# Kernel optimization log

Hardware: AMD Instinct MI355X
Metric: run time of the kernel (lower is better)

Reference implementation:

```python
import jax, jax.numpy as jnp
import numpy as np

# Straight-through-estimator round (round_pass in the original code)
def _round_ste(x):
    return x + jax.lax.stop_gradient(jnp.round(x) - x)

INPUT_QMAX = 127.0   # 2**(input_bit-1)-1,  input_bit=8
WEIGHT_QMAX = 127.0  # 2**(weight_bit-1)-1, weight_bit=8
OUT_RANGE = 127.0    # 2**(output_bit-1)-1, output_bit=8


def setup_inputs() -> dict:
    key = jax.random.key(0)
    k0, k1, k2 = jax.random.split(key, 3)
    B, Cin, Cout, H, W, K = 16, 320, 320, 64, 64, 3
    x = jax.random.normal(k0, (B, Cin, H, W), dtype=jnp.float32)
    weight = jax.random.normal(k1, (Cout, Cin, K, K), dtype=jnp.float32) * 0.05
    bias = jax.random.normal(k2, (Cout,), dtype=jnp.float32) * 0.1
    # LSQ learned scalar step sizes (cloned from conv_lsq in the original)
    step_x = jnp.float32(0.02)
    step_w = jnp.float32(0.002)
    step_b = jnp.float32(0.01)
    # Bit_shift_layer scale: shift conv accumulator down into output_bit range
    shift_scale = jnp.float32(2.0 ** -7)
    return {"x": x, "weight": weight, "bias": bias, "step_x": step_x,
            "step_w": step_w, "step_b": step_b, "shift_scale": shift_scale}


def reference(x, weight, bias, step_x, step_w, step_b, shift_scale):
    # --- lsq_quant_input (isint=True): x_int in [-127,127], x_scale = 1/step ---
    x_int = jnp.clip(_round_ste(x / step_x), -INPUT_QMAX, INPUT_QMAX)
    x_scale = 1.0 / step_x
    # --- lsq_quant_weight (isint=True) ---
    w_int = jnp.clip(_round_ste(weight / step_w), -WEIGHT_QMAX, WEIGHT_QMAX)
    w_scale = 1.0 / step_w
    # --- Conv2d_int: integer-valued conv (no bias) ---
    y_int = jax.lax.conv_general_dilated(
        x_int, w_int, window_strides=(1, 1), padding=((1, 1), (1, 1)),
        dimension_numbers=("NCHW", "OIHW", "NCHW"))
    # --- mvm_result_shift: bit-shift accumulator into output range ---
    y_shift = jnp.clip(_round_ste(y_int * shift_scale), -OUT_RANGE, OUT_RANGE)
    # --- lsq_quant_bias (isint=False): dequantized bias ---
    b_deq = jnp.clip(_round_ste(bias / step_b), -OUT_RANGE, OUT_RANGE) * step_b
    # --- bias requant to output int scale, add, clamp (fused epilogue) ---
    b_int8 = jnp.clip(_round_ste(b_deq * shift_scale * x_scale * w_scale),
                      -OUT_RANGE, OUT_RANGE)
    y_shift_dmac = jnp.clip(y_shift + b_int8[None, :, None, None],
                            -OUT_RANGE, OUT_RANGE)
    # module returns y_shift_DMAC (the integer-valued clamped output)
    return y_shift_dmac
```

## Files before the change

kernel.cpp:

```cpp
#include <hip/hip_runtime.h>

typedef int v4i __attribute__((ext_vector_type(4)));

#define QMAX 127.0f

#define XQ_BYTES 22302720
#define WQ_BYTES 921600

__device__ __forceinline__ float clampf(float v, float lo, float hi) {
    return fminf(fmaxf(v, lo), hi);
}

__device__ __forceinline__ void gload_lds16(const char* g, char* l) {
    __builtin_amdgcn_global_load_lds(
        (const __attribute__((address_space(1))) void*)g,
        (__attribute__((address_space(3))) void*)l, 16, 0, 0);
}

__global__ __launch_bounds__(256) void quant_x_kernel(
    const float* __restrict__ x, const float* __restrict__ step_p,
    char* __restrict__ xq)
{
    __shared__ float F[64 * 65];
    const int t   = threadIdx.x;
    const int ci0 = blockIdx.x * 64;
    const int h   = blockIdx.y;
    const int b   = blockIdx.z;
    const float step = *step_p;

    {
        const int r = t >> 2, q = t & 3;
        const float* src = x + (((size_t)(b * 320 + ci0 + r) * 64 + h) * 64);
#pragma unroll
        for (int i = 0; i < 4; ++i) {
            float4 v = *(const float4*)(src + q * 16 + i * 4);
            float* dst = &F[r * 65 + q * 16 + i * 4];
            dst[0] = v.x; dst[1] = v.y; dst[2] = v.z; dst[3] = v.w;
        }
    }
    __syncthreads();

    {
        const int w  = t & 63;
        const int cg = t >> 6;
        int dws[4];
#pragma unroll
        for (int j = 0; j < 4; ++j) {
            int word = 0;
#pragma unroll
            for (int k2 = 0; k2 < 4; ++k2) {
                int ci = cg * 16 + j * 4 + k2;
                float v = F[ci * 65 + w];
                int xi = (int)clampf(rintf(v / step), -QMAX, QMAX);
                word |= (xi & 0xFF) << (8 * k2);
            }
            dws[j] = word;
        }
        v4i pk = { dws[0], dws[1], dws[2], dws[3] };
        size_t off = ((size_t)(b * 66 + (h + 1)) * 66 + (w + 1)) * 320 + ci0 + cg * 16;
        *(v4i*)&xq[off] = pk;
    }
}

__global__ __launch_bounds__(256) void halo_kernel(char* __restrict__ xq)
{
    int tid = blockIdx.x * 256 + threadIdx.x;
    if (tid >= 83200) return;
    int b = tid / 5200;
    int r = tid - b * 5200;
    int px = r / 20;
    int ck = (r - px * 20) * 16;
    int row, col;
    if (px < 66)       { row = 0;  col = px; }
    else if (px < 132) { row = 65; col = px - 66; }
    else { int e = px - 132; row = 1 + (e >> 1); col = (e & 1) * 65; }
    size_t off = ((size_t)(b * 66 + row) * 66 + col) * 320 + ck;
    v4i z = {0, 0, 0, 0};
    *(v4i*)&xq[off] = z;
}

__global__ __launch_bounds__(256) void quant_w_kernel(
    const float* __restrict__ w, const float* __restrict__ step_p,
    char* __restrict__ wq2)
{
    int tid = blockIdx.x * 256 + threadIdx.x;
    const float step = *step_p;
    int co = tid / 320;
    int ci = tid - co * 320;
    int c5 = ci >> 6, quad = (ci >> 4) & 3, j = ci & 15;
    int cog = co >> 4, l15 = co & 15;
    const float* src = w + (size_t)co * 2880 + ci * 9;
    size_t base = ((size_t)(c5 * 20 + cog) * 64 + (l15 + quad * 16)) * 16 + j;
#pragma unroll
    for (int p = 0; p < 9; ++p) {
        float v = src[p];
        int q = (int)clampf(rintf(v / step), -QMAX, QMAX);
        wq2[p * 102400 + base] = (char)q;
    }
}

__global__ void quant_b_kernel(
    const float* __restrict__ bias, const float* __restrict__ step_b_p,
    const float* __restrict__ step_x_p, const float* __restrict__ step_w_p,
    const float* __restrict__ shift_p, float* __restrict__ bi)
{
    const int co = threadIdx.x;
    if (co >= 320) return;
    const float step_b = *step_b_p;
    const float xs = 1.0f / *step_x_p;
    const float ws = 1.0f / *step_w_p;
    const float shift = *shift_p;
    float b_deq = clampf(rintf(bias[co] / step_b), -QMAX, QMAX) * step_b;
    float v = ((b_deq * shift) * xs) * ws;
    bi[co] = clampf(rintf(v), -QMAX, QMAX);
}

__global__ __launch_bounds__(256) void conv_mfma_kernel(
    const char* __restrict__ xq, const char* __restrict__ wq2,
    const float* __restrict__ bi, const float* __restrict__ shift_p,
    float* __restrict__ out)
{
    __shared__ __attribute__((aligned(16))) char A_lds[36864];
    __shared__ __attribute__((aligned(16))) char B_lds[25344];

    const int t   = threadIdx.x;
    const int bx  = blockIdx.x;
    const int co0 = bx * 64;
    const int ptile = blockIdx.y;
    const int b  = ptile >> 4;
    const int h0 = (ptile & 15) * 4;

    const int wave = t >> 6, lane = t & 63;
    const int quad = lane >> 4, l15 = lane & 15;

    const char* xbase = xq + ((size_t)(b * 66 + h0) * 66) * 320;

    v4i acc[4][4] = {};

    for (int c5 = 0; c5 < 5; ++c5) {
        const int ci0 = c5 * 64;

        for (int c = t; c < 1584; c += 256) {
            int px = c >> 2;
            int ck = (c & 3) << 4;
            v4i v = *(const v4i*)&xbase[(size_t)px * 320 + ci0 + ck];
            *(v4i*)&B_lds[px * 64 + (ck ^ ((((px >> 1) & 3)) << 4))] = v;
        }

        {
            const char* g = wq2 + ((size_t)(c5 * 20 + bx * 4 + wave)) * 1024
                            + (size_t)lane * 16;
            char* l = &A_lds[wave * 1024];
#pragma unroll
            for (int p = 0; p < 9; ++p)
                gload_lds16(g + (size_t)p * 102400, l + p * 4096);
        }

        __syncthreads();

#pragma unroll
        for (int p = 0; p < 9; ++p) {
            const int dh = p / 3, dw = p - dh * 3;
            v4i a[4], bf[4];
#pragma unroll
            for (int cs = 0; cs < 4; ++cs)
                a[cs] = *(const v4i*)&A_lds[(p * 4 + cs) * 1024 + lane * 16];
#pragma unroll
            for (int i = 0; i < 4; ++i) {
                int px = (wave + dh) * 66 + i * 16 + l15 + dw;
                bf[i] = *(const v4i*)&B_lds[px * 64 +
                         ((quad << 4) ^ (((px >> 1) & 3) << 4))];
            }
#pragma unroll
            for (int cs = 0; cs < 4; ++cs)
#pragma unroll
                for (int i = 0; i < 4; ++i)
                    acc[cs][i] = __builtin_amdgcn_mfma_i32_16x16x64_i8(
                        a[cs], bf[i], acc[cs][i], 0, 0, 0);
        }

        __syncthreads();
    }

    const float shift = *shift_p;
    const int h = h0 + wave;
#pragma unroll
    for (int cs = 0; cs < 4; ++cs) {
#pragma unroll
        for (int reg = 0; reg < 4; ++reg) {
            const int co = co0 + cs * 16 + quad * 4 + reg;
            const float bv = bi[co];
            float* orow = out + (((size_t)(b * 320 + co) * 64) + h) * 64;
#pragma unroll
            for (int i = 0; i < 4; ++i) {
                float y  = (float)acc[cs][i][reg];
                float ys = clampf(rintf(y * shift), -QMAX, QMAX);
                orow[i * 16 + l15] = clampf(ys + bv, -QMAX, QMAX);
            }
        }
    }
}

extern "C" void kernel_launch(void* const* d_in, const int* in_sizes, int n_in,
                              void* d_out, int out_size, void* d_ws, size_t ws_size,
                              hipStream_t stream) {
    const float* x      = (const float*)d_in[0];
    const float* w      = (const float*)d_in[1];
    const float* bias   = (const float*)d_in[2];
    const float* step_x = (const float*)d_in[3];
    const float* step_w = (const float*)d_in[4];
    const float* step_b = (const float*)d_in[5];
    const float* shift  = (const float*)d_in[6];
    float* out = (float*)d_out;

    char*  xq  = (char*)d_ws;
    char*  wq2 = xq + XQ_BYTES;
    float* bi  = (float*)(wq2 + WQ_BYTES);

    quant_x_kernel<<<dim3(5, 64, 16), 256, 0, stream>>>(x, step_x, xq);
    halo_kernel<<<325, 256, 0, stream>>>(xq);
    quant_w_kernel<<<400, 256, 0, stream>>>(w, step_w, wq2);
    quant_b_kernel<<<1, 320, 0, stream>>>(bias, step_b, step_x, step_w, shift, bi);
    conv_mfma_kernel<<<dim3(5, 256), 256, 0, stream>>>(xq, wq2, bi, shift, out);
}
```

Measured before the change: 238.4 us.

## Double rows per conv tile, merge prep kernels, coalesce quant_x loads

```diff
diff --git a/kernel.cpp b/kernel.cpp
--- a/kernel.cpp
+++ b/kernel.cpp
@@ -15,6 +15,10 @@
     __builtin_amdgcn_global_load_lds(
         (const __attribute__((address_space(1))) void*)g,
         (__attribute__((address_space(3))) void*)l, 16, 0, 0);
+}
+
+__device__ __forceinline__ v4i mfma_i8(v4i a, v4i b, v4i c) {
+    return __builtin_amdgcn_mfma_i32_16x16x64_i8(a, b, c, 0, 0, 0);
 }
 
 __global__ __launch_bounds__(256) void quant_x_kernel(
@@ -29,13 +33,13 @@
     const float step = *step_p;
 
     {
-        const int r = t >> 2, q = t & 3;
-        const float* src = x + (((size_t)(b * 320 + ci0 + r) * 64 + h) * 64);
+        const int r = t >> 4, c = (t & 15) * 4;
+        const float* src = x + (((size_t)(b * 320 + ci0) * 64 + h) * 64);
 #pragma unroll
         for (int i = 0; i < 4; ++i) {
-            float4 v = *(const float4*)(src + q * 16 + i * 4);
-            float* dst = &F[r * 65 + q * 16 + i * 4];
-            dst[0] = v.x; dst[1] = v.y; dst[2] = v.z; dst[3] = v.w;
+            const int row = r + i * 16;
+            float4 v = *(const float4*)(src + (size_t)row * 4096 + c);
+            *(float4*)&F[row * 65 + c] = v;
         }
     }
     __syncthreads();
@@ -62,140 +66,142 @@
     }
 }
 
-__global__ __launch_bounds__(256) void halo_kernel(char* __restrict__ xq)
+__global__ __launch_bounds__(256) void prep_kernel(
+    const float* __restrict__ w, const float* __restrict__ bias,
+    const float* __restrict__ step_w_p, const float* __restrict__ step_b_p,
+    const float* __restrict__ step_x_p, const float* __restrict__ shift_p,
+    char* __restrict__ wq2, char* __restrict__ xq, float* __restrict__ bi)
 {
-    int tid = blockIdx.x * 256 + threadIdx.x;
-    if (tid >= 83200) return;
-    int b = tid / 5200;
-    int r = tid - b * 5200;
-    int px = r / 20;
-    int ck = (r - px * 20) * 16;
-    int row, col;
-    if (px < 66)       { row = 0;  col = px; }
-    else if (px < 132) { row = 65; col = px - 66; }
-    else { int e = px - 132; row = 1 + (e >> 1); col = (e & 1) * 65; }
-    size_t off = ((size_t)(b * 66 + row) * 66 + col) * 320 + ck;
-    v4i z = {0, 0, 0, 0};
-    *(v4i*)&xq[off] = z;
-}
-
-__global__ __launch_bounds__(256) void quant_w_kernel(
-    const float* __restrict__ w, const float* __restrict__ step_p,
-    char* __restrict__ wq2)
-{
-    int tid = blockIdx.x * 256 + threadIdx.x;
-    const float step = *step_p;
-    int co = tid / 320;
-    int ci = tid - co * 320;
-    int c5 = ci >> 6, quad = (ci >> 4) & 3, j = ci & 15;
-    int cog = co >> 4, l15 = co & 15;
-    const float* src = w + (size_t)co * 2880 + ci * 9;
-    size_t base = ((size_t)(c5 * 20 + cog) * 64 + (l15 + quad * 16)) * 16 + j;
-#pragma unroll
-    for (int p = 0; p < 9; ++p) {
-        float v = src[p];
+    const int bid = blockIdx.x;
+    if (bid < 3600) {
+        const int tid = bid * 256 + threadIdx.x;
+        const float step = *step_w_p;
+        const int p    = tid / 102400;
+        const int r    = tid - p * 102400;
+        const int c5   = r / 20480;
+        const int r2   = r - c5 * 20480;
+        const int cog  = r2 >> 10;
+        const int r3   = r2 & 1023;
+        const int lane = r3 >> 4, j = r3 & 15;
+        const int co = cog * 16 + (lane & 15);
+        const int ci = c5 * 64 + (lane >> 4) * 16 + j;
+        float v = w[(size_t)co * 2880 + ci * 9 + p];
         int q = (int)clampf(rintf(v / step), -QMAX, QMAX);
-        wq2[p * 102400 + base] = (char)q;
-    }
-}
-
-__global__ void quant_b_kernel(
-    const float* __restrict__ bias, const float* __restrict__ step_b_p,
-    const float* __restrict__ step_x_p, const float* __restrict__ step_w_p,
-    const float* __restrict__ shift_p, float* __restrict__ bi)
-{
-    const int co = threadIdx.x;
-    if (co >= 320) return;
-    const float step_b = *step_b_p;
-    const float xs = 1.0f / *step_x_p;
-    const float ws = 1.0f / *step_w_p;
-    const float shift = *shift_p;
-    float b_deq = clampf(rintf(bias[co] / step_b), -QMAX, QMAX) * step_b;
-    float v = ((b_deq * shift) * xs) * ws;
-    bi[co] = clampf(rintf(v), -QMAX, QMAX);
-}
-
-__global__ __launch_bounds__(256) void conv_mfma_kernel(
+        wq2[tid] = (char)q;
+    } else if (bid < 3925) {
+        int tid = (bid - 3600) * 256 + threadIdx.x;
+        if (tid < 83200) {
+            int b = tid / 5200;
+            int r = tid - b * 5200;
+            int px = r / 20;
+            int ck = (r - px * 20) * 16;
+            int row, col;
+            if (px < 66)       { row = 0;  col = px; }
+            else if (px < 132) { row = 65; col = px - 66; }
+            else { int e = px - 132; row = 1 + (e >> 1); col = (e & 1) * 65; }
+            size_t off = ((size_t)(b * 66 + row) * 66 + col) * 320 + ck;
+            v4i z = {0, 0, 0, 0};
+            *(v4i*)&xq[off] = z;
+        }
+    } else {
+        const float step_b = *step_b_p;
+        const float xs = 1.0f / *step_x_p;
+        const float ws = 1.0f / *step_w_p;
+        const float shift = *shift_p;
+#pragma unroll
+        for (int co = threadIdx.x; co < 320; co += 256) {
+            float b_deq = clampf(rintf(bias[co] / step_b), -QMAX, QMAX) * step_b;
+            float v = ((b_deq * shift) * xs) * ws;
+            bi[co] = clampf(rintf(v), -QMAX, QMAX);
+        }
+    }
+}
+
+template<int ROWS, int WAVES>
+__global__ __launch_bounds__(WAVES * 64, 2) void conv_mfma_kernel(
     const char* __restrict__ xq, const char* __restrict__ wq2,
     const float* __restrict__ bi, const float* __restrict__ shift_p,
     float* __restrict__ out)
 {
-    __shared__ __attribute__((aligned(16))) char A_lds[36864];
-    __shared__ __attribute__((aligned(16))) char B_lds[25344];
+    extern __shared__ __align__(16) char lds[];
+    char* B_lds = lds;
+    char* A_lds = lds + (ROWS + 2) * 66 * 64;
 
     const int t   = threadIdx.x;
     const int bx  = blockIdx.x;
     const int co0 = bx * 64;
     const int ptile = blockIdx.y;
-    const int b  = ptile >> 4;
-    const int h0 = (ptile & 15) * 4;
+    constexpr int TPI = 64 / ROWS;
+    const int b  = ptile / TPI;
+    const int h0 = (ptile % TPI) * ROWS;
 
     const int wave = t >> 6, lane = t & 63;
     const int quad = lane >> 4, l15 = lane & 15;
 
     const char* xbase = xq + ((size_t)(b * 66 + h0) * 66) * 320;
-
-    v4i acc[4][4] = {};
+    constexpr int BCHUNKS = (ROWS + 2) * 66 * 4;
+
+    v4i acc[4][8] = {};
 
     for (int c5 = 0; c5 < 5; ++c5) {
         const int ci0 = c5 * 64;
 
-        for (int c = t; c < 1584; c += 256) {
+        for (int c = t; c < BCHUNKS; c += WAVES * 64) {
             int px = c >> 2;
             int ck = (c & 3) << 4;
             v4i v = *(const v4i*)&xbase[(size_t)px * 320 + ci0 + ck];
             *(v4i*)&B_lds[px * 64 + (ck ^ ((((px >> 1) & 3)) << 4))] = v;
         }
-
-        {
-            const char* g = wq2 + ((size_t)(c5 * 20 + bx * 4 + wave)) * 1024
+        for (int seg = wave; seg < 36; seg += WAVES) {
+            int p = seg >> 2, cog = seg & 3;
+            const char* g = wq2 + (size_t)p * 102400
+                            + ((size_t)(c5 * 20 + bx * 4 + cog)) * 1024
                             + (size_t)lane * 16;
-            char* l = &A_lds[wave * 1024];
-#pragma unroll
-            for (int p = 0; p < 9; ++p)
-                gload_lds16(g + (size_t)p * 102400, l + p * 4096);
-        }
-
+            gload_lds16(g, &A_lds[seg * 1024]);
+        }
         __syncthreads();
 
 #pragma unroll
         for (int p = 0; p < 9; ++p) {
             const int dh = p / 3, dw = p - dh * 3;
-            v4i a[4], bf[4];
+            v4i a[4];
 #pragma unroll
             for (int cs = 0; cs < 4; ++cs)
                 a[cs] = *(const v4i*)&A_lds[(p * 4 + cs) * 1024 + lane * 16];
 #pragma unroll
-            for (int i = 0; i < 4; ++i) {
-                int px = (wave + dh) * 66 + i * 16 + l15 + dw;
-                bf[i] = *(const v4i*)&B_lds[px * 64 +
-                         ((quad << 4) ^ (((px >> 1) & 3) << 4))];
+            for (int half = 0; half < 2; ++half) {
+                const int prow = wave * 2 + half + dh;
+#pragma unroll
+                for (int i = 0; i < 4; ++i) {
+                    const int px = prow * 66 + i * 16 + l15 + dw;
+                    v4i bf = *(const v4i*)&B_lds[px * 64 +
+                              ((quad << 4) ^ ((((px >> 1) & 3)) << 4))];
+#pragma unroll
+                    for (int cs = 0; cs < 4; ++cs)
+                        acc[cs][half * 4 + i] = mfma_i8(a[cs], bf, acc[cs][half * 4 + i]);
+                }
             }
-#pragma unroll
-            for (int cs = 0; cs < 4; ++cs)
-#pragma unroll
-                for (int i = 0; i < 4; ++i)
-                    acc[cs][i] = __builtin_amdgcn_mfma_i32_16x16x64_i8(
-                        a[cs], bf[i], acc[cs][i], 0, 0, 0);
-        }
-
+        }
         __syncthreads();
     }
 
     const float shift = *shift_p;
-    const int h = h0 + wave;
 #pragma unroll
     for (int cs = 0; cs < 4; ++cs) {
 #pragma unroll
         for (int reg = 0; reg < 4; ++reg) {
             const int co = co0 + cs * 16 + quad * 4 + reg;
             const float bv = bi[co];
-            float* orow = out + (((size_t)(b * 320 + co) * 64) + h) * 64;
-#pragma unroll
-            for (int i = 0; i < 4; ++i) {
-                float y  = (float)acc[cs][i][reg];
-                float ys = clampf(rintf(y * shift), -QMAX, QMAX);
-                orow[i * 16 + l15] = clampf(ys + bv, -QMAX, QMAX);
+#pragma unroll
+            for (int half = 0; half < 2; ++half) {
+                const int h = h0 + wave * 2 + half;
+                float* orow = out + (((size_t)(b * 320 + co) * 64) + h) * 64;
+#pragma unroll
+                for (int i = 0; i < 4; ++i) {
+                    float y  = (float)acc[cs][half * 4 + i][reg];
+                    float ys = clampf(rintf(y * shift), -QMAX, QMAX);
+                    orow[i * 16 + l15] = clampf(ys + bv, -QMAX, QMAX);
+                }
             }
         }
     }
@@ -218,8 +224,20 @@
     float* bi  = (float*)(wq2 + WQ_BYTES);
 
     quant_x_kernel<<<dim3(5, 64, 16), 256, 0, stream>>>(x, step_x, xq);
-    halo_kernel<<<325, 256, 0, stream>>>(xq);
-    quant_w_kernel<<<400, 256, 0, stream>>>(w, step_w, wq2);
-    quant_b_kernel<<<1, 320, 0, stream>>>(bias, step_b, step_x, step_w, shift, bi);
-    conv_mfma_kernel<<<dim3(5, 256), 256, 0, stream>>>(xq, wq2, bi, shift, out);
-}
+    prep_kernel<<<3926, 256, 0, stream>>>(w, bias, step_w, step_b, step_x, shift,
+                                          wq2, xq, bi);
+
+    const int lds_big = (8 + 2) * 66 * 64 + 36864;
+    hipError_t e = hipFuncSetAttribute(
+        reinterpret_cast<const void*>(&conv_mfma_kernel<8, 4>),
+        hipFuncAttributeMaxDynamicSharedMemorySize, lds_big);
+    if (e == hipSuccess) {
+        conv_mfma_kernel<8, 4><<<dim3(5, 128), 256, lds_big, stream>>>(
+            xq, wq2, bi, shift, out);
+    } else {
+        (void)hipGetLastError();
+        const int lds_small = (4 + 2) * 66 * 64 + 36864;
+        conv_mfma_kernel<4, 2><<<dim3(5, 256), 128, lds_small, stream>>>(
+            xq, wq2, bi, shift, out);
+    }
+}
```

Measured after the change: 236.7 us. No clear change (-0.7%).
